# Kernel tuning notes

Measured on AMD Instinct MI355X. Metric: run time of the kernel, lower is better.

The kernel has to match this reference:

```python
import jax, jax.numpy as jnp
import numpy as np

SQUARE_SIZE = 32
BATCH, CH, H, W = 256, 3, 224, 224


def setup_inputs() -> dict:
    key = jax.random.key(0)
    k1, k2, k3 = jax.random.split(key, 3)
    img = jax.random.normal(k1, (BATCH, CH, H, W), dtype=jnp.float32)
    hi = H - SQUARE_SIZE + 1  # 193
    y_idx = jax.random.randint(k2, (BATCH,), 0, hi, dtype=jnp.int32)
    x_idx = jax.random.randint(k3, (BATCH,), 0, hi, dtype=jnp.int32)
    return {"img": img, "y_idx": y_idx, "x_idx": x_idx}


def reference(img, y_idx, x_idx):
    # img: [B, C, H, W]; y_idx/x_idx: [B] top-left corners of zeroed square.
    B, C, H, W = img.shape
    rows = jnp.arange(H, dtype=jnp.int32)  # [H]
    cols = jnp.arange(W, dtype=jnp.int32)  # [W]
    # in_y: [B, H], in_x: [B, W]
    in_y = (rows[None, :] >= y_idx[:, None]) & (rows[None, :] < y_idx[:, None] + SQUARE_SIZE)
    in_x = (cols[None, :] >= x_idx[:, None]) & (cols[None, :] < x_idx[:, None] + SQUARE_SIZE)
    # square region -> mask 0, else 1; broadcast over channels
    in_square = in_y[:, None, :, None] & in_x[:, None, None, :]  # [B, 1, H, W]
    mask = jnp.where(in_square, jnp.float32(0.0), jnp.float32(1.0))
    return img * mask
```

## Files before the change

kernel.cpp:

```cpp
#include <hip/hip_runtime.h>


#define SQ 32
#define B_ 256
#define C_ 3
#define H_ 224
#define W_ 224

#define W4 (W_ / 4)
#define PLANE4 (H_ * W4)
#define SPLIT 7
#define CHUNK4 (PLANE4 / SPLIT)
#define TPB 256
#define ITERS (CHUNK4 / TPB)

typedef float v4f __attribute__((ext_vector_type(4)));

__global__ __launch_bounds__(TPB) void rsd_kernel(const v4f* __restrict__ img,
                                                  const int* __restrict__ y_idx,
                                                  const int* __restrict__ x_idx,
                                                  v4f* __restrict__ out) {
    const int blk   = (int)blockIdx.x;
    const int plane = blk / SPLIT;
    const int chunk = blk - plane * SPLIT;
    const int b     = plane / C_;

    const int y0 = y_idx[b];
    const int x0 = x_idx[b];

    const int t     = (int)threadIdx.x;
    const int base4 = plane * PLANE4 + chunk * CHUNK4 + t;

    v4f v[ITERS];
#pragma unroll
    for (int k = 0; k < ITERS; ++k)
        v[k] = img[base4 + k * TPB];

    __builtin_amdgcn_sched_barrier(0);

#pragma unroll
    for (int k = 0; k < ITERS; ++k) {
        const int o4 = chunk * CHUNK4 + k * TPB + t;
        const int h  = o4 / W4;
        const int w  = (o4 - h * W4) << 2;
        const int cx = w - x0;
        if ((unsigned)(h - y0) < SQ) {
            if ((unsigned)(cx + 0) < SQ) v[k].x = 0.0f;
            if ((unsigned)(cx + 1) < SQ) v[k].y = 0.0f;
            if ((unsigned)(cx + 2) < SQ) v[k].z = 0.0f;
            if ((unsigned)(cx + 3) < SQ) v[k].w = 0.0f;
        }
        out[base4 + k * TPB] = v[k];
    }
}

extern "C" void kernel_launch(void* const* d_in, const int* in_sizes, int n_in,
                              void* d_out, int out_size, void* d_ws, size_t ws_size,
                              hipStream_t stream) {
    const v4f* img  = (const v4f*)d_in[0];
    const int* yidx = (const int*)d_in[1];
    const int* xidx = (const int*)d_in[2];
    v4f*       out  = (v4f*)d_out;

    rsd_kernel<<<dim3(B_ * C_ * SPLIT), TPB, 0, stream>>>(img, yidx, xidx, out);
}
```

Baseline: 262.6 us.

## Process three chunks per block with a hand-scheduled rolling load/store pipeline

Each block now handles three plane chunks instead of one, and the grid shrinks to a third. Loads are issued through inline assembly into a four-deep register ring, with explicit vmcnt waits so stores of earlier elements overlap with loads still in flight. The aim is fewer blocks and a steady stream of outstanding memory operations rather than a burst of loads followed by a burst of stores. The hand-written waitcnt accounting is fragile: stores also increment vmcnt, so the wait thresholds must be exactly right, and fewer outstanding loads per thread could lower memory-level parallelism.

Result: slower. 268.4 us (+2.2%).

```diff
diff --git a/kernel.cpp b/kernel.cpp
--- a/kernel.cpp
+++ b/kernel.cpp
@@ -12,46 +12,93 @@
 #define SPLIT 7
 #define CHUNK4 (PLANE4 / SPLIT)
 #define TPB 256
-#define ITERS (CHUNK4 / TPB)
 
 typedef float v4f __attribute__((ext_vector_type(4)));
+
+template <int N>
+__device__ __forceinline__ void vwait() {
+    static_assert(N >= 3 && N <= 6, "window");
+    if constexpr (N == 3) asm volatile("s_waitcnt vmcnt(3)" ::: "memory");
+    else if constexpr (N == 4) asm volatile("s_waitcnt vmcnt(4)" ::: "memory");
+    else if constexpr (N == 5) asm volatile("s_waitcnt vmcnt(5)" ::: "memory");
+    else                       asm volatile("s_waitcnt vmcnt(6)" ::: "memory");
+    __builtin_amdgcn_sched_barrier(0);
+}
 
 __global__ __launch_bounds__(TPB) void rsd_kernel(const v4f* __restrict__ img,
                                                   const int* __restrict__ y_idx,
                                                   const int* __restrict__ x_idx,
                                                   v4f* __restrict__ out) {
-    const int blk   = (int)blockIdx.x;
-    const int plane = blk / SPLIT;
-    const int chunk = blk - plane * SPLIT;
-    const int b     = plane / C_;
+    const int blk = (int)blockIdx.x;
+    const int t   = (int)threadIdx.x;
 
-    const int y0 = y_idx[b];
-    const int x0 = x_idx[b];
+    int base4[3], y0a[3], x0a[3], coff[3];
+#pragma unroll
+    for (int j = 0; j < 3; ++j) {
+        const int u     = blk * 3 + j;
+        const int plane = u / SPLIT;
+        const int chunk = u - plane * SPLIT;
+        const int b     = plane / C_;
+        y0a[j]   = y_idx[b];
+        x0a[j]   = x_idx[b];
+        coff[j]  = chunk * CHUNK4;
+        base4[j] = plane * PLANE4 + coff[j] + t;
+    }
 
-    const int t     = (int)threadIdx.x;
-    const int base4 = plane * PLANE4 + chunk * CHUNK4 + t;
+    v4f vb[4];
 
-    v4f v[ITERS];
-#pragma unroll
-    for (int k = 0; k < ITERS; ++k)
-        v[k] = img[base4 + k * TPB];
+#define ISSUE(K)                                                           \
+    {                                                                      \
+        constexpr int j_ = (K) / 7, it_ = (K) % 7;                         \
+        asm volatile("global_load_dwordx4 %0, %1, off"                     \
+                     : "=v"(vb[(K) & 3])                                   \
+                     : "v"(img + base4[j_] + it_ * TPB)                    \
+                     : "memory");                                          \
+    }
 
-    __builtin_amdgcn_sched_barrier(0);
+#define CONSUME(K)                                                         \
+    {                                                                      \
+        constexpr int j_ = (K) / 7, it_ = (K) % 7;                         \
+        vwait<((20 - (K)) < 3 ? (20 - (K)) : 3) + ((K) < 3 ? (K) : 3)>();  \
+        v4f v = vb[(K) & 3];                                               \
+        const int o4 = coff[j_] + it_ * TPB + t;                           \
+        const int h  = o4 / W4;                             \
+        const int w  = (o4 - h * W4) << 2;                                 \
+        const int cx = w - x0a[j_];                                        \
+        if ((unsigned)(h - y0a[j_]) < SQ) {                                \
+            if ((unsigned)(cx + 0) < SQ) v.x = 0.0f;                       \
+            if ((unsigned)(cx + 1) < SQ) v.y = 0.0f;                       \
+            if ((unsigned)(cx + 2) < SQ) v.z = 0.0f;                       \
+            if ((unsigned)(cx + 3) < SQ) v.w = 0.0f;                       \
+        }                                                                  \
+        out[base4[j_] + it_ * TPB] = v;                                    \
+    }
 
-#pragma unroll
-    for (int k = 0; k < ITERS; ++k) {
-        const int o4 = chunk * CHUNK4 + k * TPB + t;
-        const int h  = o4 / W4;
-        const int w  = (o4 - h * W4) << 2;
-        const int cx = w - x0;
-        if ((unsigned)(h - y0) < SQ) {
-            if ((unsigned)(cx + 0) < SQ) v[k].x = 0.0f;
-            if ((unsigned)(cx + 1) < SQ) v[k].y = 0.0f;
-            if ((unsigned)(cx + 2) < SQ) v[k].z = 0.0f;
-            if ((unsigned)(cx + 3) < SQ) v[k].w = 0.0f;
-        }
-        out[base4 + k * TPB] = v[k];
-    }
+    ISSUE(0) ISSUE(1) ISSUE(2) ISSUE(3)
+    CONSUME(0)  ISSUE(4)
+    CONSUME(1)  ISSUE(5)
+    CONSUME(2)  ISSUE(6)
+    CONSUME(3)  ISSUE(7)
+    CONSUME(4)  ISSUE(8)
+    CONSUME(5)  ISSUE(9)
+    CONSUME(6)  ISSUE(10)
+    CONSUME(7)  ISSUE(11)
+    CONSUME(8)  ISSUE(12)
+    CONSUME(9)  ISSUE(13)
+    CONSUME(10) ISSUE(14)
+    CONSUME(11) ISSUE(15)
+    CONSUME(12) ISSUE(16)
+    CONSUME(13) ISSUE(17)
+    CONSUME(14) ISSUE(18)
+    CONSUME(15) ISSUE(19)
+    CONSUME(16) ISSUE(20)
+    CONSUME(17)
+    CONSUME(18)
+    CONSUME(19)
+    CONSUME(20)
+
+#undef ISSUE
+#undef CONSUME
 }
 
 extern "C" void kernel_launch(void* const* d_in, const int* in_sizes, int n_in,
@@ -62,5 +109,5 @@
     const int* xidx = (const int*)d_in[2];
     v4f*       out  = (v4f*)d_out;
 
-    rsd_kernel<<<dim3(B_ * C_ * SPLIT), TPB, 0, stream>>>(img, yidx, xidx, out);
+    rsd_kernel<<<dim3(1792), TPB, 0, stream>>>(img, yidx, xidx, out);
 }
```
